# Kernel optimization log

Measured on AMD Instinct MI355X. Metric: run time of the kernel, lower is better.

Reference implementation:

```python
import jax, jax.numpy as jnp
import numpy as np

V, E, H, M = 256, 512, 512, 128
D = 2 * H  # decoder hidden
B, L_TXT, T_MEL = 32, 256, 800
EPS = 1e-5


def setup_inputs() -> dict:
    key = jax.random.key(0)
    ks = jax.random.split(key, 24)
    s = 0.02
    inp = {
        'x': jax.random.randint(ks[0], (B, L_TXT), 0, V),
        'text_seq_lens': jax.random.randint(ks[1], (B,), 1, L_TXT + 1),
        'y': jax.random.normal(ks[2], (B, T_MEL, M), jnp.float32),
        'mel_spec_lens': jax.random.randint(ks[3], (B,), 1, T_MEL + 1),
        'emb': jax.random.normal(ks[4], (V, E)) * s,
        'conv1_w': jax.random.normal(ks[5], (E, E, 3)) * s,
        'conv1_b': jnp.zeros((E,)),
        'bn1_g': jnp.ones((E,)), 'bn1_b': jnp.zeros((E,)),
        'conv2_w': jax.random.normal(ks[6], (E, E, 3)) * s,
        'conv2_b': jnp.zeros((E,)),
        'bn2_g': jnp.ones((E,)), 'bn2_b': jnp.zeros((E,)),
        'wih_f': jax.random.normal(ks[7], (4 * H, E)) * s,
        'whh_f': jax.random.normal(ks[8], (4 * H, H)) * s,
        'bih_f': jnp.zeros((4 * H,)), 'bhh_f': jnp.zeros((4 * H,)),
        'wih_b': jax.random.normal(ks[9], (4 * H, E)) * s,
        'whh_b': jax.random.normal(ks[10], (4 * H, H)) * s,
        'bih_b': jnp.zeros((4 * H,)), 'bhh_b': jnp.zeros((4 * H,)),
        'dwih': jax.random.normal(ks[11], (4 * D, M)) * s,
        'dwhh': jax.random.normal(ks[12], (4 * D, D)) * s,
        'dbih': jnp.zeros((4 * D,)), 'dbhh': jnp.zeros((4 * D,)),
        'proj_w': jax.random.normal(ks[13], (M, D)) * s,
        'proj_b': jnp.zeros((M,)),
        'gate_w': jax.random.normal(ks[14], (1, D)) * s,
        'gate_b': jnp.zeros((1,)),
    }
    return inp


def _conv_bn_relu(x, w, b, g, beta):
    # x: (B, E, L); training-mode BatchNorm (batch statistics, biased var)
    x = jax.lax.conv_general_dilated(x, w, (1,), [(1, 1)],
                                     dimension_numbers=('NCH', 'OIH', 'NCH')) + b[None, :, None]
    mu = jnp.mean(x, axis=(0, 2), keepdims=True)
    var = jnp.mean((x - mu) ** 2, axis=(0, 2), keepdims=True)
    x = (x - mu) * jax.lax.rsqrt(var + EPS) * g[None, :, None] + beta[None, :, None]
    return jax.nn.relu(x)


def _lstm_last(xseq, lens, wih, whh, bih, bhh):
    # Run LSTM over full padded seq, freezing state past each length.
    # Returns final (h, c) == state at t = len-1 (packed-sequence semantics).
    Bb, T, _ = xseq.shape
    Hh = whh.shape[1]
    pre = jnp.einsum('bte,ge->btg', xseq, wih) + bih + bhh  # (B,T,4H)

    def step(carry, inp):
        h, c = carry
        xt, t = inp
        gates = xt + h @ whh.T
        i, f, g, o = jnp.split(gates, 4, axis=-1)
        c_n = jax.nn.sigmoid(f) * c + jax.nn.sigmoid(i) * jnp.tanh(g)
        h_n = jax.nn.sigmoid(o) * jnp.tanh(c_n)
        valid = (t < lens)[:, None]
        return (jnp.where(valid, h_n, h), jnp.where(valid, c_n, c)), None

    init = (jnp.zeros((Bb, Hh), xseq.dtype), jnp.zeros((Bb, Hh), xseq.dtype))
    (h, c), _ = jax.lax.scan(step, init, (pre.transpose(1, 0, 2), jnp.arange(T)))
    return h, c


def _forward(x, text_seq_lens, y, mel_spec_lens, emb, conv1_w, conv1_b, bn1_g, bn1_b,
             conv2_w, conv2_b, bn2_g, bn2_b, wih_f, whh_f, bih_f, bhh_f,
             wih_b, whh_b, bih_b, bhh_b, dwih, dwhh, dbih, dbhh,
             proj_w, proj_b, gate_w, gate_b):
    xe = emb[x]                       # (B, L, E)
    h = xe.transpose(0, 2, 1)         # (B, E, L)
    h = _conv_bn_relu(h, conv1_w, conv1_b, bn1_g, bn1_b)  # dropout = identity (eval)
    h = _conv_bn_relu(h, conv2_w, conv2_b, bn2_g, bn2_b)
    h = h.transpose(0, 2, 1)          # (B, L, E)

    # bidirectional encoder LSTM final states (packed semantics)
    hf, cf = _lstm_last(h, text_seq_lens, wih_f, whh_f, bih_f, bhh_f)
    # reverse each sequence within its valid length for the backward direction
    t_idx = jnp.arange(h.shape[1])[None, :]
    rev_idx = jnp.clip(text_seq_lens[:, None] - 1 - t_idx, 0, h.shape[1] - 1)
    h_rev = jnp.take_along_axis(h, rev_idx[:, :, None], axis=1)
    hb, cb = _lstm_last(h_rev, text_seq_lens, wih_b, whh_b, bih_b, bhh_b)

    hid = jnp.concatenate([hf, hb], axis=1)  # (B, 2H)
    cel = jnp.concatenate([cf, cb], axis=1)

    Tm = y.shape[1]

    def dec_step(carry, _):
        hd, cd, inp = carry
        gates = inp @ dwih.T + dbih + dbhh + hd @ dwhh.T
        i, f, g, o = jnp.split(gates, 4, axis=-1)
        cd = jax.nn.sigmoid(f) * cd + jax.nn.sigmoid(i) * jnp.tanh(g)
        hd = jax.nn.sigmoid(o) * jnp.tanh(cd)
        mel = hd @ proj_w.T + proj_b          # (B, M)
        gate = hd @ gate_w.T + gate_b         # (B, 1)
        return (hd, cd, mel), (mel, gate[:, 0])

    sos = jnp.zeros((y.shape[0], M), y.dtype)
    _, (mels, gates) = jax.lax.scan(dec_step, (hid, cel, sos), None, length=Tm)
    mel_outputs = mels.transpose(1, 0, 2)     # (B, Tm, M)
    gate_outputs = gates.T                    # (B, Tm)

    mask = jnp.arange(Tm)[None, :] > mel_spec_lens[:, None]  # (B, Tm), strictly >
    masked_mel = jnp.where(mask[:, :, None], 0.0, mel_outputs)
    masked_gate = jnp.where(mask, 1000.0, gate_outputs)
    return masked_mel, masked_gate, mask


def reference(x, text_seq_lens, y, mel_spec_lens, emb, conv1_w, conv1_b, bn1_g, bn1_b,
              conv2_w, conv2_b, bn2_g, bn2_b, wih_f, whh_f, bih_f, bhh_f,
              wih_b, whh_b, bih_b, bhh_b, dwih, dwhh, dbih, dbhh,
              proj_w, proj_b, gate_w, gate_b):
    return _forward(x, text_seq_lens, y, mel_spec_lens, emb, conv1_w, conv1_b,
                    bn1_g, bn1_b, conv2_w, conv2_b, bn2_g, bn2_b,
                    wih_f, whh_f, bih_f, bhh_f, wih_b, whh_b, bih_b, bhh_b,
                    dwih, dwhh, dbih, dbhh, proj_w, proj_b, gate_w, gate_b)
```

## Files before the change

kernel.cpp:

```cpp
#include <hip/hip_runtime.h>


typedef float f4 __attribute__((ext_vector_type(4)));
typedef _Float16 h8 __attribute__((ext_vector_type(8)));
typedef _Float16 half_t;
typedef unsigned u4 __attribute__((ext_vector_type(4)));
typedef unsigned long long u64;

#define B_    32
#define LTXT  256
#define TMEL  800
#define EE    512
#define HH    512
#define DD    1024
#define MM    128
#define NROWS 8192
#define GATE_OFF 3276800
#define MASK_OFF 3302400

#define RING_D 101
#define RING_E 33
#define HOP    13

#define WS_MBE        0ull
#define WS_MBD        16384ull
#define WS_HENC       49152ull
#define WS_ZERO_BYTES 114688ull
#define WS_HD         2211840ull
#define WS_BUFX       8830976ull
#define WS_BUFY       17219584ull
#define WS_CONVF      25608192ull
#define WS_WEFF       25608192ull
#define WS_W0         33996800ull
#define WS_WP1        42385408ull
#define WS_WP2        43958272ull
#define WS_WIHP       45531136ull
#define WS_WHHP       49725440ull
#define WS_BSUM       53919744ull
#define WS_BEFF       53936128ull
#define WS_B0         53952512ull
#define WS_MEAN       53968896ull
#define WS_RSTD       53970944ull
#define WS_PROJW      53972992ull
#define WS_PROJG      54235136ull
#define WS_CEL        54267904ull

__device__ __forceinline__ float sigm(float x) { return 1.f / (1.f + __expf(-x)); }
__device__ __forceinline__ float tanh_f(float x) {
    float e = __expf(2.f * x);
    return 1.f - 2.f / (e + 1.f);
}

__device__ __forceinline__ void st_atom64(void* p, u64 v) {
    asm volatile("global_atomic_swap_x2 %0, %1, off" :: "v"(p), "v"(v) : "memory");
}
__device__ __forceinline__ void st_atom32(unsigned* p, unsigned v) {
    asm volatile("global_atomic_swap %0, %1, off" :: "v"(p), "v"(v) : "memory");
}
__device__ __forceinline__ u4 ld_l3(const void* p) {
    u4 r;
    asm volatile("global_load_dwordx4 %0, %1, off sc0 sc1" : "=v"(r) : "v"(p) : "memory");
    return r;
}
__device__ __forceinline__ void wait_vm0() {
    asm volatile("s_waitcnt vmcnt(0)" ::: "memory");
    __builtin_amdgcn_sched_barrier(0);
}


__global__ void k_embed(const int* __restrict__ x, const float* __restrict__ emb,
                        half_t* __restrict__ out) {
    int row = blockIdx.x;
    int tok = x[row];
    const float* e = emb + (size_t)tok * EE;
    half_t* o = out + (size_t)row * EE;
    for (int c = threadIdx.x; c < EE; c += blockDim.x) o[c] = (half_t)e[c];
}

__global__ void k_packconvw(const float* __restrict__ w, half_t* __restrict__ wp) {
    int idx = blockIdx.x * 256 + threadIdx.x;
    if (idx >= 3 * EE * EE) return;
    int s = idx / (EE * EE);
    int rem = idx - s * EE * EE;
    int eo = rem >> 9, ei = rem & 511;
    wp[idx] = (half_t)w[(size_t)eo * (EE * 3) + ei * 3 + s];
}

__global__ __launch_bounds__(256) void k_conv(const half_t* __restrict__ A,
                                              const half_t* __restrict__ Wp,
                                              const float* __restrict__ bias,
                                              float* __restrict__ out) {
    const int nt = blockIdx.x, et = blockIdx.y;
    const int tid = threadIdx.x;
    const int wv = tid >> 6, l = tid & 63, quad = l >> 4, lo = l & 15;
    const int rowA = nt * 64 + wv * 16 + lo;
    const int eo = et * 16 + lo;
    f4 acc = {0.f, 0.f, 0.f, 0.f};
    for (int s = 0; s < 3; ++s) {
        int lsp = (rowA & 255) + s - 1;
        bool valid = (lsp >= 0) && (lsp < 256);
        int rs = rowA + s - 1;
        rs = rs < 0 ? 0 : (rs > NROWS - 1 ? NROWS - 1 : rs);
        const half_t* ab = A + (size_t)rs * EE;
        const half_t* wb = Wp + ((size_t)s * EE + eo) * EE;
#pragma unroll 4
        for (int ks = 0; ks < 16; ++ks) {
            h8 a = {0, 0, 0, 0, 0, 0, 0, 0};
            if (valid) a = *(const h8*)(ab + ks * 32 + quad * 8);
            h8 b = *(const h8*)(wb + ks * 32 + quad * 8);
            acc = __builtin_amdgcn_mfma_f32_16x16x32_f16(a, b, acc, 0, 0, 0);
        }
    }
    const int orow = nt * 64 + wv * 16 + quad * 4;
    const float bv = bias[eo];
#pragma unroll
    for (int r = 0; r < 4; ++r) out[(size_t)(orow + r) * EE + eo] = acc[r] + bv;
}

__global__ __launch_bounds__(256) void k_bnstats(const float* __restrict__ x,
                                                 float* __restrict__ mean,
                                                 float* __restrict__ rstd) {
    const int c = blockIdx.x;
    float s = 0.f, ss = 0.f;
    for (int n = threadIdx.x; n < NROWS; n += 256) {
        float v = x[(size_t)n * EE + c];
        s += v; ss += v * v;
    }
#pragma unroll
    for (int off = 32; off > 0; off >>= 1) { s += __shfl_down(s, off); ss += __shfl_down(ss, off); }
    __shared__ float as[4], ass[4];
    int wv = threadIdx.x >> 6;
    if ((threadIdx.x & 63) == 0) { as[wv] = s; ass[wv] = ss; }
    __syncthreads();
    if (threadIdx.x == 0) {
        float S = as[0] + as[1] + as[2] + as[3];
        float SS = ass[0] + ass[1] + ass[2] + ass[3];
        float m = S / (float)NROWS;
        float var = SS / (float)NROWS - m * m;
        mean[c] = m;
        rstd[c] = rsqrtf(var + 1e-5f);
    }
}

__global__ void k_bnapply(const float* __restrict__ x, const float* __restrict__ mean,
                          const float* __restrict__ rstd, const float* __restrict__ g,
                          const float* __restrict__ beta, half_t* __restrict__ out) {
    int idx = blockIdx.x * 256 + threadIdx.x;
    if (idx >= NROWS * EE) return;
    int c = idx & (EE - 1);
    float v = (x[idx] - mean[c]) * rstd[c] * g[c] + beta[c];
    out[idx] = (half_t)(v > 0.f ? v : 0.f);
}

__global__ void k_packrec(const float* __restrict__ src, half_t* __restrict__ dst,
                          int Hdim, int kshift, int total) {
    int idx = blockIdx.x * 256 + threadIdx.x;
    if (idx >= total) return;
    int p = idx >> kshift;
    int k = idx & ((1 << kshift) - 1);
    int he = p >> 2, g = p & 3;
    dst[idx] = (half_t)src[((size_t)g * Hdim + he) * (size_t)(1 << kshift) + k];
}

__global__ void k_bsumenc(const float* __restrict__ bf, const float* __restrict__ bhf,
                          const float* __restrict__ bb, const float* __restrict__ bhb,
                          float* __restrict__ bsum) {
    int p = blockIdx.x * 256 + threadIdx.x;
    if (p >= 4096) return;
    int dir = p >> 11, pp = p & 2047;
    int he = pp >> 2, g = pp & 3;
    int row = g * HH + he;
    bsum[p] = dir ? (bb[row] + bhb[row]) : (bf[row] + bhf[row]);
}

__global__ __launch_bounds__(256) void k_weff(const float* __restrict__ dwhh,
                                              const float* __restrict__ dwih,
                                              const float* __restrict__ projw,
                                              half_t* __restrict__ weff,
                                              half_t* __restrict__ w0) {
    int row = blockIdx.x;
    int k = blockIdx.y * 256 + threadIdx.x;
    float v = dwhh[(size_t)row * DD + k];
    float acc = v;
    for (int m = 0; m < MM; ++m) acc += dwih[(size_t)row * MM + m] * projw[(size_t)m * DD + k];
    int p = ((row & (DD - 1)) << 2) | (row >> 10);
    weff[(size_t)p * DD + k] = (half_t)acc;
    w0[(size_t)p * DD + k] = (half_t)v;
}

__global__ void k_bdec(const float* __restrict__ dbih, const float* __restrict__ dbhh,
                       const float* __restrict__ dwih, const float* __restrict__ projb,
                       float* __restrict__ beff, float* __restrict__ b0) {
    int p = blockIdx.x * 256 + threadIdx.x;
    if (p >= 4096) return;
    int he = p >> 2, g = p & 3;
    int row = g * DD + he;
    float bb = dbih[row] + dbhh[row];
    float acc = bb;
    for (int m = 0; m < MM; ++m) acc += dwih[(size_t)row * MM + m] * projb[m];
    b0[p] = bb;
    beff[p] = acc;
}

__global__ void k_cast(const float* __restrict__ src, half_t* __restrict__ dst, int n) {
    int idx = blockIdx.x * 256 + threadIdx.x;
    if (idx < n) dst[idx] = (half_t)src[idx];
}

__global__ void k_projg(const float* __restrict__ gw, half_t* __restrict__ pg) {
    int idx = blockIdx.x * 256 + threadIdx.x;
    if (idx >= 16 * DD) return;
    int row = idx >> 10, k = idx & (DD - 1);
    pg[idx] = (half_t)(row == 0 ? gw[k] : 0.f);
}

__global__ void k_mask(const int* __restrict__ lens, float* __restrict__ out) {
    int idx = blockIdx.x * 256 + threadIdx.x;
    if (idx >= B_ * TMEL) return;
    int b = idx / TMEL, t = idx - b * TMEL;
    out[MASK_OFF + idx] = (t > lens[b]) ? 1.f : 0.f;
}

__global__ __launch_bounds__(512) void k_enc(const half_t* __restrict__ X,
                                             const half_t* __restrict__ wihp,
                                             const half_t* __restrict__ whhp,
                                             const float* __restrict__ bsum,
                                             const int* __restrict__ lens,
                                             half_t* __restrict__ henc,
                                             half_t* __restrict__ hd0,
                                             float* __restrict__ cel,
                                             unsigned* __restrict__ mbE) {
    const int j = blockIdx.x;
    const int dir = j >> 5, sub = j & 31;
    const int tid = threadIdx.x;
    const int wv = tid >> 6, l = tid & 63, quad = l >> 4, lo = l & 15;
    const int rg = wv >> 1, bh = wv & 1;
    const int bfr = bh * 16 + lo;
    const int ue = tid >> 5, ub = tid & 31;

    __shared__ half_t s_hd[32 * 520];
    __shared__ float s_g[32][65];
    __shared__ float s_c[16][32];
    __shared__ float s_h[16][32];
    __shared__ half_t s_hh[16][32];
    __shared__ int s_len[32];

    if (tid < 32) s_len[tid] = lens[tid];
    s_c[ue][ub] = 0.f;
    s_h[ue][ub] = 0.f;

    const int pr = dir * 2048 + sub * 64 + rg * 16 + lo;
    const half_t* wih_b = wihp + (size_t)pr * 512;
    const half_t* whh_b = whhp + (size_t)pr * 512;
    const float bias_n = bsum[pr];

    h8 wihreg[16], whhreg[16];
#pragma unroll
    for (int ks = 0; ks < 16; ++ks) {
        wihreg[ks] = *(const h8*)(wih_b + ks * 32 + quad * 8);
        whhreg[ks] = *(const h8*)(whh_b + ks * 32 + quad * 8);
    }

    int sp = 0, sn = HOP;
    __syncthreads();

    for (int t = 0; t < 256; ++t) {
        if (t > 0) {
            if (tid >= 64 && tid < 96) {
                const unsigned want = (unsigned)t;
                const unsigned* fp = mbE + (size_t)(dir * 32 + sub) * 64 + (tid - 64);
                while (__hip_atomic_load(fp, __ATOMIC_RELAXED, __HIP_MEMORY_SCOPE_AGENT) < want)
                    __builtin_amdgcn_s_sleep(1);
            }
            __syncthreads();
        }

        const half_t* src = henc + (size_t)sp * 32768 + (size_t)dir * 16384;
        u4 tmp0 = ld_l3(src + (size_t)(tid + 0 * 512) * 8);
        u4 tmp1 = ld_l3(src + (size_t)(tid + 1 * 512) * 8);
        u4 tmp2 = ld_l3(src + (size_t)(tid + 2 * 512) * 8);
        u4 tmp3 = ld_l3(src + (size_t)(tid + 3 * 512) * 8);

        const int lb = s_len[bfr];
        int tt = (dir == 0) ? t : (lb - 1 - t);
        tt = tt < 0 ? 0 : tt;
        const half_t* xr = X + ((size_t)bfr * 256 + tt) * 512;
        f4 accA = {0.f, 0.f, 0.f, 0.f}, accB = {0.f, 0.f, 0.f, 0.f};
#pragma unroll
        for (int ks = 0; ks < 16; ++ks) {
            h8 a = *(const h8*)(xr + ks * 32 + quad * 8);
            accA = __builtin_amdgcn_mfma_f32_16x16x32_f16(a, wihreg[ks], accA, 0, 0, 0);
        }

        wait_vm0();
        {
            int c0 = tid;
            *(u4*)(s_hd + (size_t)(c0 >> 6) * 520 + (c0 & 63) * 8) = tmp0;
            int c1 = tid + 512;
            *(u4*)(s_hd + (size_t)(c1 >> 6) * 520 + (c1 & 63) * 8) = tmp1;
            int c2 = tid + 1024;
            *(u4*)(s_hd + (size_t)(c2 >> 6) * 520 + (c2 & 63) * 8) = tmp2;
            int c3 = tid + 1536;
            *(u4*)(s_hd + (size_t)(c3 >> 6) * 520 + (c3 & 63) * 8) = tmp3;
        }
        __syncthreads();

#pragma unroll
        for (int ks = 0; ks < 16; ++ks) {
            h8 a = *(const h8*)(s_hd + (size_t)bfr * 520 + ks * 32 + quad * 8);
            accB = __builtin_amdgcn_mfma_f32_16x16x32_f16(a, whhreg[ks], accB, 0, 0, 0);
        }
        const int bm = bh * 16 + quad * 4, cm = rg * 16 + lo;
#pragma unroll
        for (int r = 0; r < 4; ++r) s_g[bm + r][cm] = accA[r] + accB[r] + bias_n;
        __syncthreads();
        {
            float gi = s_g[ub][ue * 4 + 0], gf = s_g[ub][ue * 4 + 1];
            float gg = s_g[ub][ue * 4 + 2], go = s_g[ub][ue * 4 + 3];
            float cn = sigm(gf) * s_c[ue][ub] + sigm(gi) * tanh_f(gg);
            float hn = sigm(go) * tanh_f(cn);
            if (t < s_len[ub]) { s_c[ue][ub] = cn; s_h[ue][ub] = hn; }
            s_hh[ue][ub] = (half_t)s_h[ue][ub];
        }
        __syncthreads();
        if (tid < 64 && t < 255) {
            int b2 = tid >> 1, e8 = (tid & 1) * 8;
            union { half_t h[8]; u64 u[2]; } pk;
#pragma unroll
            for (int i = 0; i < 8; ++i) pk.h[i] = s_hh[e8 + i][b2];
            half_t* dst = henc + (size_t)sn * 32768 + (size_t)dir * 16384
                          + (size_t)b2 * 512 + sub * 16 + e8;
            st_atom64(dst, pk.u[0]);
            st_atom64(dst + 4, pk.u[1]);
            asm volatile("s_waitcnt vmcnt(0)");
            if (tid < 32)
                st_atom32(mbE + ((size_t)(dir * 32 + tid) * 64 + sub), (unsigned)(t + 1));
        }
        if (t < 255) { sp = sn; sn += HOP; if (sn >= RING_E) sn -= RING_E; }
    }
    hd0[(size_t)ub * 1024 + dir * 512 + sub * 16 + ue] = (half_t)s_h[ue][ub];
    cel[(size_t)ub * 1024 + dir * 512 + sub * 16 + ue] = s_c[ue][ub];
}

__global__ __launch_bounds__(512) void k_dec(const half_t* __restrict__ Weff,
                                             const half_t* __restrict__ W0,
                                             const float* __restrict__ beff,
                                             const float* __restrict__ b0,
                                             const half_t* __restrict__ projwb,
                                             const half_t* __restrict__ projg,
                                             const float* __restrict__ projb,
                                             const float* __restrict__ gateb,
                                             const int* __restrict__ mlens,
                                             const float* __restrict__ cel,
                                             half_t* __restrict__ hd,
                                             float* __restrict__ out,
                                             unsigned* __restrict__ mbD) {
    const int j = blockIdx.x;
    const int tid = threadIdx.x;
    const int wv = tid >> 6, l = tid & 63, quad = l >> 4, lo = l & 15;

    __shared__ half_t s_hd[32 * 1032];
    __shared__ float s_g[32][65];
    __shared__ float s_c[16][32];
    __shared__ half_t s_hh[16][32];
    __shared__ int s_len[32];

    if (j < 64) {
        const int rg = wv >> 1, bh = wv & 1;
        const int bfr = bh * 16 + lo;
        const int ue = tid >> 5, ub = tid & 31;

        s_c[ue][ub] = cel[(size_t)ub * 1024 + j * 16 + ue];
        const int pr = j * 64 + rg * 16 + lo;
        const float biasE = beff[pr], bias0 = b0[pr];
        const half_t* wbE = Weff + (size_t)pr * 1024;
        const half_t* wb0 = W0 + (size_t)pr * 1024;

        h8 wreg[32];
#pragma unroll
        for (int ks = 0; ks < 32; ++ks)
            wreg[ks] = *(const h8*)(wbE + ks * 32 + quad * 8);

        int sp = 0, sn = HOP;
        __syncthreads();

        for (int t = 1; t <= TMEL; ++t) {
            if (t > 1) {
                if (tid >= 64 && tid < 128) {
                    const unsigned want = (unsigned)(t - 1);
                    const unsigned* fp = mbD + (size_t)j * 64 + (tid - 64);
                    while (__hip_atomic_load(fp, __ATOMIC_RELAXED, __HIP_MEMORY_SCOPE_AGENT) < want)
                        __builtin_amdgcn_s_sleep(1);
                }
                __syncthreads();
            }

            {
                const half_t* src = hd + (size_t)sp * 32768;
                u4 tp[8];
#pragma unroll
                for (int i = 0; i < 8; ++i)
                    tp[i] = ld_l3(src + (size_t)(tid + i * 512) * 8);
                wait_vm0();
#pragma unroll
                for (int i = 0; i < 8; ++i) {
                    int c = tid + i * 512;
                    *(u4*)(s_hd + (size_t)(c >> 7) * 1032 + (c & 127) * 8) = tp[i];
                }
            }
            __syncthreads();

            const half_t* ar = s_hd + (size_t)bfr * 1032 + quad * 8;
            f4 acc = {0.f, 0.f, 0.f, 0.f}, acc2 = {0.f, 0.f, 0.f, 0.f};
            if (t == 1) {
#pragma unroll 8
                for (int ks = 0; ks < 32; ks += 2) {
                    h8 a0 = *(const h8*)(ar + ks * 32);
                    h8 a1 = *(const h8*)(ar + ks * 32 + 32);
                    acc = __builtin_amdgcn_mfma_f32_16x16x32_f16(a0, *(const h8*)(wb0 + ks * 32 + quad * 8), acc, 0, 0, 0);
                    acc2 = __builtin_amdgcn_mfma_f32_16x16x32_f16(a1, *(const h8*)(wb0 + ks * 32 + 32 + quad * 8), acc2, 0, 0, 0);
                }
            } else {
#pragma unroll
                for (int ks = 0; ks < 32; ks += 2) {
                    h8 a0 = *(const h8*)(ar + ks * 32);
                    h8 a1 = *(const h8*)(ar + ks * 32 + 32);
                    acc = __builtin_amdgcn_mfma_f32_16x16x32_f16(a0, wreg[ks], acc, 0, 0, 0);
                    acc2 = __builtin_amdgcn_mfma_f32_16x16x32_f16(a1, wreg[ks + 1], acc2, 0, 0, 0);
                }
            }
            const float bn = (t == 1) ? bias0 : biasE;
            const int bm = bh * 16 + quad * 4, cm = rg * 16 + lo;
#pragma unroll
            for (int r = 0; r < 4; ++r) s_g[bm + r][cm] = acc[r] + acc2[r] + bn;
            __syncthreads();
            {
                float gi = s_g[ub][ue * 4 + 0], gf = s_g[ub][ue * 4 + 1];
                float gg = s_g[ub][ue * 4 + 2], go = s_g[ub][ue * 4 + 3];
                float cn = sigm(gf) * s_c[ue][ub] + sigm(gi) * tanh_f(gg);
                s_c[ue][ub] = cn;
                s_hh[ue][ub] = (half_t)(sigm(go) * tanh_f(cn));
            }
            __syncthreads();
            if (tid < 64) {
                int b2 = tid >> 1, e8 = (tid & 1) * 8;
                union { half_t h[8]; u64 u[2]; } pk;
#pragma unroll
                for (int i = 0; i < 8; ++i) pk.h[i] = s_hh[e8 + i][b2];
                half_t* dst = hd + (size_t)sn * 32768 + (size_t)b2 * 1024 + j * 16 + e8;
                st_atom64(dst, pk.u[0]);
                st_atom64(dst + 4, pk.u[1]);
                asm volatile("s_waitcnt vmcnt(0)");
                st_atom32(mbD + ((size_t)tid * 64 + j), (unsigned)t);
                if (tid < 9)
                    st_atom32(mbD + ((size_t)(64 + tid) * 64 + j), (unsigned)t);
            }
            sp = sn; sn += HOP; if (sn >= RING_D) sn -= RING_D;
        }
    } else {
        const int pj = j - 64;
        const bool meld = (pj < 8);
        const bool duty = (wv < 2);
        const int bh2 = wv & 1;
        const half_t* pw = meld ? (projwb + (size_t)(pj * 16 + lo) * 1024)
                                : (projg + (size_t)lo * 1024);
        const float biasP = meld ? projb[pj * 16 + lo] : gateb[0];

        h8 pwreg[32];
        if (duty) {
#pragma unroll
            for (int ks = 0; ks < 32; ++ks)
                pwreg[ks] = *(const h8*)(pw + ks * 32 + quad * 8);
        }
        if (tid < 32) s_len[tid] = mlens[tid];

        int spP = HOP;
        __syncthreads();

        for (int t = 1; t <= TMEL; ++t) {
            if (tid < 64) {
                const unsigned want = (unsigned)t;
                const unsigned* fp = mbD + (size_t)(64 + pj) * 64 + tid;
                while (__hip_atomic_load(fp, __ATOMIC_RELAXED, __HIP_MEMORY_SCOPE_AGENT) < want)
                    __builtin_amdgcn_s_sleep(1);
            }
            __syncthreads();

            {
                const half_t* src = hd + (size_t)spP * 32768;
                u4 tp[8];
#pragma unroll
                for (int i = 0; i < 8; ++i)
                    tp[i] = ld_l3(src + (size_t)(tid + i * 512) * 8);
                wait_vm0();
#pragma unroll
                for (int i = 0; i < 8; ++i) {
                    int c = tid + i * 512;
                    *(u4*)(s_hd + (size_t)(c >> 7) * 1032 + (c & 127) * 8) = tp[i];
                }
            }
            __syncthreads();

            if (duty) {
                const half_t* ar = s_hd + (size_t)(bh2 * 16 + lo) * 1032 + quad * 8;
                f4 accm = {0.f, 0.f, 0.f, 0.f}, accm2 = {0.f, 0.f, 0.f, 0.f};
#pragma unroll
                for (int ks = 0; ks < 32; ks += 2) {
                    h8 a0 = *(const h8*)(ar + ks * 32);
                    h8 a1 = *(const h8*)(ar + ks * 32 + 32);
                    accm = __builtin_amdgcn_mfma_f32_16x16x32_f16(a0, pwreg[ks], accm, 0, 0, 0);
                    accm2 = __builtin_amdgcn_mfma_f32_16x16x32_f16(a1, pwreg[ks + 1], accm2, 0, 0, 0);
                }
                accm[0] += accm2[0]; accm[1] += accm2[1];
                accm[2] += accm2[2]; accm[3] += accm2[3];
                const int pos = t - 1;
                if (meld) {
#pragma unroll
                    for (int r = 0; r < 4; ++r) {
                        int b = bh2 * 16 + quad * 4 + r;
                        float v = accm[r] + biasP;
                        if (pos > s_len[b]) v = 0.f;
                        __builtin_nontemporal_store(v,
                            &out[(size_t)b * (TMEL * MM) + (size_t)pos * MM + pj * 16 + lo]);
                    }
                } else if (lo == 0) {
#pragma unroll
                    for (int r = 0; r < 4; ++r) {
                        int b = bh2 * 16 + quad * 4 + r;
                        float v = accm[r] + biasP;
                        if (pos > s_len[b]) v = 1000.f;
                        __builtin_nontemporal_store(v, &out[GATE_OFF + (size_t)b * TMEL + pos]);
                    }
                }
            }
            __syncthreads();
            spP += HOP; if (spP >= RING_D) spP -= RING_D;
        }
    }
}


extern "C" void kernel_launch(void* const* d_in, const int* in_sizes, int n_in,
                              void* d_out, int out_size, void* d_ws, size_t ws_size,
                              hipStream_t stream) {
    const int* x = (const int*)d_in[0];
    const int* tlens = (const int*)d_in[1];
    const int* mlens = (const int*)d_in[3];
    const float* emb = (const float*)d_in[4];
    const float* c1w = (const float*)d_in[5];
    const float* c1b = (const float*)d_in[6];
    const float* bn1g = (const float*)d_in[7];
    const float* bn1b = (const float*)d_in[8];
    const float* c2w = (const float*)d_in[9];
    const float* c2b = (const float*)d_in[10];
    const float* bn2g = (const float*)d_in[11];
    const float* bn2b = (const float*)d_in[12];
    const float* wihf = (const float*)d_in[13];
    const float* whhf = (const float*)d_in[14];
    const float* bihf = (const float*)d_in[15];
    const float* bhhf = (const float*)d_in[16];
    const float* wihb = (const float*)d_in[17];
    const float* whhb = (const float*)d_in[18];
    const float* bihb = (const float*)d_in[19];
    const float* bhhb = (const float*)d_in[20];
    const float* dwih = (const float*)d_in[21];
    const float* dwhh = (const float*)d_in[22];
    const float* dbih = (const float*)d_in[23];
    const float* dbhh = (const float*)d_in[24];
    const float* projw = (const float*)d_in[25];
    const float* projb = (const float*)d_in[26];
    const float* gatew = (const float*)d_in[27];
    const float* gateb = (const float*)d_in[28];
    float* out = (float*)d_out;
    char* ws = (char*)d_ws;

    unsigned* mbE = (unsigned*)(ws + WS_MBE);
    unsigned* mbD = (unsigned*)(ws + WS_MBD);
    half_t* henc = (half_t*)(ws + WS_HENC);
    half_t* hd = (half_t*)(ws + WS_HD);
    half_t* bufX = (half_t*)(ws + WS_BUFX);
    half_t* bufY = (half_t*)(ws + WS_BUFY);
    float* convf = (float*)(ws + WS_CONVF);
    half_t* weff = (half_t*)(ws + WS_WEFF);
    half_t* w0 = (half_t*)(ws + WS_W0);
    half_t* wp1 = (half_t*)(ws + WS_WP1);
    half_t* wp2 = (half_t*)(ws + WS_WP2);
    float* meanb = (float*)(ws + WS_MEAN);
    float* rstdb = (float*)(ws + WS_RSTD);
    half_t* wihp = (half_t*)(ws + WS_WIHP);
    half_t* whhp = (half_t*)(ws + WS_WHHP);
    float* bsum = (float*)(ws + WS_BSUM);
    float* beff = (float*)(ws + WS_BEFF);
    float* b0 = (float*)(ws + WS_B0);
    half_t* projwb = (half_t*)(ws + WS_PROJW);
    half_t* projg = (half_t*)(ws + WS_PROJG);
    float* cel = (float*)(ws + WS_CEL);

    hipMemsetAsync(d_ws, 0, (size_t)WS_ZERO_BYTES, stream);

    k_embed<<<NROWS, 256, 0, stream>>>(x, emb, bufX);
    k_packconvw<<<(3 * EE * EE + 255) / 256, 256, 0, stream>>>(c1w, wp1);
    k_conv<<<dim3(128, 32), 256, 0, stream>>>(bufX, wp1, c1b, convf);
    k_bnstats<<<EE, 256, 0, stream>>>(convf, meanb, rstdb);
    k_bnapply<<<(NROWS * EE) / 256, 256, 0, stream>>>(convf, meanb, rstdb, bn1g, bn1b, bufY);
    k_packconvw<<<(3 * EE * EE + 255) / 256, 256, 0, stream>>>(c2w, wp2);
    k_conv<<<dim3(128, 32), 256, 0, stream>>>(bufY, wp2, c2b, convf);
    k_bnstats<<<EE, 256, 0, stream>>>(convf, meanb, rstdb);
    k_bnapply<<<(NROWS * EE) / 256, 256, 0, stream>>>(convf, meanb, rstdb, bn2g, bn2b, bufX);

    const int encTot = 2048 * 512;
    k_packrec<<<(encTot + 255) / 256, 256, 0, stream>>>(wihf, wihp, HH, 9, encTot);
    k_packrec<<<(encTot + 255) / 256, 256, 0, stream>>>(wihb, wihp + encTot, HH, 9, encTot);
    k_packrec<<<(encTot + 255) / 256, 256, 0, stream>>>(whhf, whhp, HH, 9, encTot);
    k_packrec<<<(encTot + 255) / 256, 256, 0, stream>>>(whhb, whhp + encTot, HH, 9, encTot);
    k_bsumenc<<<16, 256, 0, stream>>>(bihf, bhhf, bihb, bhhb, bsum);

    k_enc<<<64, 512, 0, stream>>>(bufX, wihp, whhp, bsum, tlens, henc, hd, cel, mbE);

    k_weff<<<dim3(4096, 4), 256, 0, stream>>>(dwhh, dwih, projw, weff, w0);
    k_bdec<<<16, 256, 0, stream>>>(dbih, dbhh, dwih, projb, beff, b0);
    k_cast<<<(MM * DD + 255) / 256, 256, 0, stream>>>(projw, projwb, MM * DD);
    k_projg<<<(16 * DD + 255) / 256, 256, 0, stream>>>(gatew, projg);

    k_dec<<<73, 512, 0, stream>>>(weff, w0, beff, b0, projwb, projg, projb, gateb,
                                  mlens, cel, hd, out, mbD);

    k_mask<<<(B_ * TMEL + 255) / 256, 256, 0, stream>>>(mlens, out);

    (void)in_sizes; (void)n_in; (void)out_size; (void)ws_size;
}
```

Baseline: 5.149 ms.

## Replace mailbox flags with epoch-tagged data words in recurrent ring buffers

The encoder and decoder recurrences now embed an epoch/timestep tag beside every 32-bit pair of hidden-state halves, and consumers spin directly on the data words. This replaces the separate per-block mailbox flags, the store-then-flag ordering wait, and the extra barrier round. The decoder's backpressure is now an explicit progress counter from the projection blocks, and ring sizes are reduced. The cost is doubling the bytes moved per step for the hidden state, plus per-element polling loops. A per-launch epoch counter avoids clearing the large ring buffers on every call.

After: 12.49 ms. 2.43x slower.

```diff
diff --git a/kernel.cpp b/kernel.cpp
--- a/kernel.cpp
+++ b/kernel.cpp
@@ -18,38 +18,41 @@
 #define GATE_OFF 3276800
 #define MASK_OFF 3302400
 
-#define RING_D 101
-#define RING_E 33
+#define RING_D 64
+#define RING_E 16
 #define HOP    13
 
-#define WS_MBE        0ull
-#define WS_MBD        16384ull
-#define WS_HENC       49152ull
-#define WS_ZERO_BYTES 114688ull
-#define WS_HD         2211840ull
-#define WS_BUFX       8830976ull
-#define WS_BUFY       17219584ull
-#define WS_CONVF      25608192ull
-#define WS_WEFF       25608192ull
-#define WS_W0         33996800ull
-#define WS_WP1        42385408ull
-#define WS_WP2        43958272ull
-#define WS_WIHP       45531136ull
-#define WS_WHHP       49725440ull
-#define WS_BSUM       53919744ull
-#define WS_BEFF       53936128ull
-#define WS_B0         53952512ull
-#define WS_MEAN       53968896ull
-#define WS_RSTD       53970944ull
-#define WS_PROJW      53972992ull
-#define WS_PROJG      54235136ull
-#define WS_CEL        54267904ull
+#define WS_PROG       0ull
+#define WS_EPOCT      4096ull
+#define WS_EPOCH      4160ull
+#define WS_HENC       8192ull
+#define WS_HD         2105344ull
+#define WS_BUFX       10493952ull
+#define WS_BUFY       18882560ull
+#define WS_CONVF      27271168ull
+#define WS_WEFF       27271168ull
+#define WS_W0         35659776ull
+#define WS_WP1        44048384ull
+#define WS_WP2        45621248ull
+#define WS_WIHP       47194112ull
+#define WS_WHHP       51388416ull
+#define WS_BSUM       55582720ull
+#define WS_BEFF       55599104ull
+#define WS_B0         55615488ull
+#define WS_MEAN       55631872ull
+#define WS_RSTD       55633920ull
+#define WS_PROJW      55635968ull
+#define WS_PROJG      55898112ull
+#define WS_CEL        55930880ull
 
 __device__ __forceinline__ float sigm(float x) { return 1.f / (1.f + __expf(-x)); }
 __device__ __forceinline__ float tanh_f(float x) {
     float e = __expf(2.f * x);
     return 1.f - 2.f / (e + 1.f);
 }
+__device__ __forceinline__ unsigned mktag(unsigned ep, int t) {
+    return (ep << 11) | (unsigned)t;
+}
 
 __device__ __forceinline__ void st_atom64(void* p, u64 v) {
     asm volatile("global_atomic_swap_x2 %0, %1, off" :: "v"(p), "v"(v) : "memory");
@@ -67,6 +70,12 @@
     __builtin_amdgcn_sched_barrier(0);
 }
 
+
+__global__ void k_epoch(unsigned long long* ctr, unsigned* cur) {
+    unsigned long long e = *ctr + 1ull;
+    *ctr = e;
+    *cur = (unsigned)e;
+}
 
 __global__ void k_embed(const int* __restrict__ x, const float* __restrict__ emb,
                         half_t* __restrict__ out) {
@@ -226,10 +235,10 @@
                                              const half_t* __restrict__ whhp,
                                              const float* __restrict__ bsum,
                                              const int* __restrict__ lens,
-                                             half_t* __restrict__ henc,
-                                             half_t* __restrict__ hd0,
+                                             u64* __restrict__ hencT,
+                                             u64* __restrict__ hdT,
                                              float* __restrict__ cel,
-                                             unsigned* __restrict__ mbE) {
+                                             const unsigned* __restrict__ epc) {
     const int j = blockIdx.x;
     const int dir = j >> 5, sub = j & 31;
     const int tid = threadIdx.x;
@@ -248,6 +257,7 @@
     if (tid < 32) s_len[tid] = lens[tid];
     s_c[ue][ub] = 0.f;
     s_h[ue][ub] = 0.f;
+    const unsigned ep = epc[0];
 
     const int pr = dir * 2048 + sub * 64 + rg * 16 + lo;
     const half_t* wih_b = wihp + (size_t)pr * 512;
@@ -265,21 +275,11 @@
     __syncthreads();
 
     for (int t = 0; t < 256; ++t) {
-        if (t > 0) {
-            if (tid >= 64 && tid < 96) {
-                const unsigned want = (unsigned)t;
-                const unsigned* fp = mbE + (size_t)(dir * 32 + sub) * 64 + (tid - 64);
-                while (__hip_atomic_load(fp, __ATOMIC_RELAXED, __HIP_MEMORY_SCOPE_AGENT) < want)
-                    __builtin_amdgcn_s_sleep(1);
-            }
-            __syncthreads();
-        }
-
-        const half_t* src = henc + (size_t)sp * 32768 + (size_t)dir * 16384;
-        u4 tmp0 = ld_l3(src + (size_t)(tid + 0 * 512) * 8);
-        u4 tmp1 = ld_l3(src + (size_t)(tid + 1 * 512) * 8);
-        u4 tmp2 = ld_l3(src + (size_t)(tid + 2 * 512) * 8);
-        u4 tmp3 = ld_l3(src + (size_t)(tid + 3 * 512) * 8);
+        const char* base = (const char*)hencT + (size_t)sp * 131072 + (size_t)dir * 65536;
+        u4 tp[8];
+#pragma unroll
+        for (int i = 0; i < 8; ++i)
+            tp[i] = ld_l3(base + ((size_t)tid + i * 512) * 16);
 
         const int lb = s_len[bfr];
         int tt = (dir == 0) ? t : (lb - 1 - t);
@@ -293,15 +293,22 @@
         }
 
         wait_vm0();
-        {
-            int c0 = tid;
-            *(u4*)(s_hd + (size_t)(c0 >> 6) * 520 + (c0 & 63) * 8) = tmp0;
-            int c1 = tid + 512;
-            *(u4*)(s_hd + (size_t)(c1 >> 6) * 520 + (c1 & 63) * 8) = tmp1;
-            int c2 = tid + 1024;
-            *(u4*)(s_hd + (size_t)(c2 >> 6) * 520 + (c2 & 63) * 8) = tmp2;
-            int c3 = tid + 1536;
-            *(u4*)(s_hd + (size_t)(c3 >> 6) * 520 + (c3 & 63) * 8) = tmp3;
+        if (t > 0) {
+            const unsigned want = mktag(ep, t);
+#pragma unroll
+            for (int i = 0; i < 8; ++i) {
+                while (tp[i][1] != want || tp[i][3] != want) {
+                    __builtin_amdgcn_s_sleep(4);
+                    tp[i] = ld_l3(base + ((size_t)tid + i * 512) * 16);
+                    wait_vm0();
+                }
+            }
+        }
+#pragma unroll
+        for (int i = 0; i < 8; ++i) {
+            int pp = tid + i * 512;
+            u64 v = ((u64)tp[i][2] << 32) | (u64)tp[i][0];
+            *(u64*)(s_hd + (size_t)(pp >> 7) * 520 + (pp & 127) * 4) = v;
         }
         __syncthreads();
 
@@ -324,21 +331,25 @@
         }
         __syncthreads();
         if (tid < 64 && t < 255) {
-            int b2 = tid >> 1, e8 = (tid & 1) * 8;
-            union { half_t h[8]; u64 u[2]; } pk;
-#pragma unroll
-            for (int i = 0; i < 8; ++i) pk.h[i] = s_hh[e8 + i][b2];
-            half_t* dst = henc + (size_t)sn * 32768 + (size_t)dir * 16384
-                          + (size_t)b2 * 512 + sub * 16 + e8;
-            st_atom64(dst, pk.u[0]);
-            st_atom64(dst + 4, pk.u[1]);
-            asm volatile("s_waitcnt vmcnt(0)");
-            if (tid < 32)
-                st_atom32(mbE + ((size_t)(dir * 32 + tid) * 64 + sub), (unsigned)(t + 1));
+            int b2 = tid >> 1, hv = tid & 1;
+            const u64 tagw = (u64)mktag(ep, t + 1) << 32;
+            u64* dstw = hencT + (size_t)sn * 16384 + (size_t)dir * 8192
+                        + (size_t)b2 * 256 + sub * 8 + hv * 4;
+#pragma unroll
+            for (int k = 0; k < 4; ++k) {
+                int e = hv * 8 + 2 * k;
+                union { half_t h[2]; unsigned u; } pk;
+                pk.h[0] = s_hh[e + 0][b2]; pk.h[1] = s_hh[e + 1][b2];
+                st_atom64(dstw + k, tagw | (u64)pk.u);
+            }
         }
         if (t < 255) { sp = sn; sn += HOP; if (sn >= RING_E) sn -= RING_E; }
     }
-    hd0[(size_t)ub * 1024 + dir * 512 + sub * 16 + ue] = (half_t)s_h[ue][ub];
+    if (!(ue & 1)) {
+        union { half_t h[2]; unsigned u; } pk;
+        pk.h[0] = (half_t)s_h[ue][ub]; pk.h[1] = (half_t)s_h[ue + 1][ub];
+        hdT[(size_t)ub * 512 + dir * 256 + sub * 8 + (ue >> 1)] = (u64)pk.u;
+    }
     cel[(size_t)ub * 1024 + dir * 512 + sub * 16 + ue] = s_c[ue][ub];
 }
 
@@ -352,12 +363,14 @@
                                              const float* __restrict__ gateb,
                                              const int* __restrict__ mlens,
                                              const float* __restrict__ cel,
-                                             half_t* __restrict__ hd,
+                                             u64* __restrict__ hdT,
                                              float* __restrict__ out,
-                                             unsigned* __restrict__ mbD) {
+                                             unsigned* __restrict__ prog,
+                                             const unsigned* __restrict__ epc) {
     const int j = blockIdx.x;
     const int tid = threadIdx.x;
     const int wv = tid >> 6, l = tid & 63, quad = l >> 4, lo = l & 15;
+    const unsigned ep = epc[0];
 
     __shared__ half_t s_hd[32 * 1032];
     __shared__ float s_g[32][65];
@@ -385,28 +398,31 @@
         __syncthreads();
 
         for (int t = 1; t <= TMEL; ++t) {
+            const char* base = (const char*)hdT + (size_t)sp * 131072;
+            u4 tp[16];
+#pragma unroll
+            for (int i = 0; i < 16; ++i)
+                tp[i] = ld_l3(base + ((size_t)tid + i * 512) * 16);
+            unsigned pv = 0x7FFFFFFFu;
+            if (tid < 9)
+                pv = __hip_atomic_load(prog + tid, __ATOMIC_RELAXED, __HIP_MEMORY_SCOPE_AGENT);
+            wait_vm0();
             if (t > 1) {
-                if (tid >= 64 && tid < 128) {
-                    const unsigned want = (unsigned)(t - 1);
-                    const unsigned* fp = mbD + (size_t)j * 64 + (tid - 64);
-                    while (__hip_atomic_load(fp, __ATOMIC_RELAXED, __HIP_MEMORY_SCOPE_AGENT) < want)
-                        __builtin_amdgcn_s_sleep(1);
-                }
-                __syncthreads();
-            }
-
-            {
-                const half_t* src = hd + (size_t)sp * 32768;
-                u4 tp[8];
-#pragma unroll
-                for (int i = 0; i < 8; ++i)
-                    tp[i] = ld_l3(src + (size_t)(tid + i * 512) * 8);
-                wait_vm0();
-#pragma unroll
-                for (int i = 0; i < 8; ++i) {
-                    int c = tid + i * 512;
-                    *(u4*)(s_hd + (size_t)(c >> 7) * 1032 + (c & 127) * 8) = tp[i];
-                }
+                const unsigned want = mktag(ep, t - 1);
+#pragma unroll
+                for (int i = 0; i < 16; ++i) {
+                    while (tp[i][1] != want || tp[i][3] != want) {
+                        __builtin_amdgcn_s_sleep(4);
+                        tp[i] = ld_l3(base + ((size_t)tid + i * 512) * 16);
+                        wait_vm0();
+                    }
+                }
+            }
+#pragma unroll
+            for (int i = 0; i < 16; ++i) {
+                int pp = tid + i * 512;
+                u64 v = ((u64)tp[i][2] << 32) | (u64)tp[i][0];
+                *(u64*)(s_hd + (size_t)(pp >> 8) * 1032 + (pp & 255) * 4) = v;
             }
             __syncthreads();
 
@@ -443,17 +459,25 @@
             }
             __syncthreads();
             if (tid < 64) {
-                int b2 = tid >> 1, e8 = (tid & 1) * 8;
-                union { half_t h[8]; u64 u[2]; } pk;
-#pragma unroll
-                for (int i = 0; i < 8; ++i) pk.h[i] = s_hh[e8 + i][b2];
-                half_t* dst = hd + (size_t)sn * 32768 + (size_t)b2 * 1024 + j * 16 + e8;
-                st_atom64(dst, pk.u[0]);
-                st_atom64(dst + 4, pk.u[1]);
-                asm volatile("s_waitcnt vmcnt(0)");
-                st_atom32(mbD + ((size_t)tid * 64 + j), (unsigned)t);
-                if (tid < 9)
-                    st_atom32(mbD + ((size_t)(64 + tid) * 64 + j), (unsigned)t);
+                if (t >= 63) {
+                    const int need = t - 62;
+                    while (!__all((int)pv >= need)) {
+                        __builtin_amdgcn_s_sleep(8);
+                        if (tid < 9)
+                            pv = __hip_atomic_load(prog + tid, __ATOMIC_RELAXED,
+                                                   __HIP_MEMORY_SCOPE_AGENT);
+                    }
+                }
+                int b2 = tid >> 1, hv = tid & 1;
+                const u64 tagw = (u64)mktag(ep, t) << 32;
+                u64* dstw = hdT + (size_t)sn * 16384 + (size_t)b2 * 512 + j * 8 + hv * 4;
+#pragma unroll
+                for (int k = 0; k < 4; ++k) {
+                    int e = hv * 8 + 2 * k;
+                    union { half_t h[2]; unsigned u; } pk;
+                    pk.h[0] = s_hh[e + 0][b2]; pk.h[1] = s_hh[e + 1][b2];
+                    st_atom64(dstw + k, tagw | (u64)pk.u);
+                }
             }
             sp = sn; sn += HOP; if (sn >= RING_D) sn -= RING_D;
         }
@@ -478,26 +502,28 @@
         __syncthreads();
 
         for (int t = 1; t <= TMEL; ++t) {
-            if (tid < 64) {
-                const unsigned want = (unsigned)t;
-                const unsigned* fp = mbD + (size_t)(64 + pj) * 64 + tid;
-                while (__hip_atomic_load(fp, __ATOMIC_RELAXED, __HIP_MEMORY_SCOPE_AGENT) < want)
-                    __builtin_amdgcn_s_sleep(1);
-            }
-            __syncthreads();
-
+            const char* base = (const char*)hdT + (size_t)spP * 131072;
+            u4 tp[16];
+#pragma unroll
+            for (int i = 0; i < 16; ++i)
+                tp[i] = ld_l3(base + ((size_t)tid + i * 512) * 16);
+            wait_vm0();
             {
-                const half_t* src = hd + (size_t)spP * 32768;
-                u4 tp[8];
-#pragma unroll
-                for (int i = 0; i < 8; ++i)
-                    tp[i] = ld_l3(src + (size_t)(tid + i * 512) * 8);
-                wait_vm0();
-#pragma unroll
-                for (int i = 0; i < 8; ++i) {
-                    int c = tid + i * 512;
-                    *(u4*)(s_hd + (size_t)(c >> 7) * 1032 + (c & 127) * 8) = tp[i];
-                }
+                const unsigned want = mktag(ep, t);
+#pragma unroll
+                for (int i = 0; i < 16; ++i) {
+                    while (tp[i][1] != want || tp[i][3] != want) {
+                        __builtin_amdgcn_s_sleep(4);
+                        tp[i] = ld_l3(base + ((size_t)tid + i * 512) * 16);
+                        wait_vm0();
+                    }
+                }
+            }
+#pragma unroll
+            for (int i = 0; i < 16; ++i) {
+                int pp = tid + i * 512;
+                u64 v = ((u64)tp[i][2] << 32) | (u64)tp[i][0];
+                *(u64*)(s_hd + (size_t)(pp >> 8) * 1032 + (pp & 255) * 4) = v;
             }
             __syncthreads();
 
@@ -534,6 +560,7 @@
                 }
             }
             __syncthreads();
+            if (tid == 0) st_atom32(prog + pj, (unsigned)t);
             spP += HOP; if (spP >= RING_D) spP -= RING_D;
         }
     }
@@ -574,10 +601,11 @@
     float* out = (float*)d_out;
     char* ws = (char*)d_ws;
 
-    unsigned* mbE = (unsigned*)(ws + WS_MBE);
-    unsigned* mbD = (unsigned*)(ws + WS_MBD);
-    half_t* henc = (half_t*)(ws + WS_HENC);
-    half_t* hd = (half_t*)(ws + WS_HD);
+    unsigned* prog = (unsigned*)(ws + WS_PROG);
+    unsigned long long* epoct = (unsigned long long*)(ws + WS_EPOCT);
+    unsigned* epc = (unsigned*)(ws + WS_EPOCH);
+    u64* hencT = (u64*)(ws + WS_HENC);
+    u64* hdT = (u64*)(ws + WS_HD);
     half_t* bufX = (half_t*)(ws + WS_BUFX);
     half_t* bufY = (half_t*)(ws + WS_BUFY);
     float* convf = (float*)(ws + WS_CONVF);
@@ -596,7 +624,9 @@
     half_t* projg = (half_t*)(ws + WS_PROJG);
     float* cel = (float*)(ws + WS_CEL);
 
-    hipMemsetAsync(d_ws, 0, (size_t)WS_ZERO_BYTES, stream);
+    hipMemsetAsync(ws + WS_PROG, 0, 4096, stream);
+    hipMemsetAsync(ws + WS_HENC, 0, 131072, stream);
+    k_epoch<<<1, 1, 0, stream>>>(epoct, epc);
 
     k_embed<<<NROWS, 256, 0, stream>>>(x, emb, bufX);
     k_packconvw<<<(3 * EE * EE + 255) / 256, 256, 0, stream>>>(c1w, wp1);
@@ -615,7 +645,7 @@
     k_packrec<<<(encTot + 255) / 256, 256, 0, stream>>>(whhb, whhp + encTot, HH, 9, encTot);
     k_bsumenc<<<16, 256, 0, stream>>>(bihf, bhhf, bihb, bhhb, bsum);
 
-    k_enc<<<64, 512, 0, stream>>>(bufX, wihp, whhp, bsum, tlens, henc, hd, cel, mbE);
+    k_enc<<<64, 512, 0, stream>>>(bufX, wihp, whhp, bsum, tlens, hencT, hdT, cel, epc);
 
     k_weff<<<dim3(4096, 4), 256, 0, stream>>>(dwhh, dwih, projw, weff, w0);
     k_bdec<<<16, 256, 0, stream>>>(dbih, dbhh, dwih, projb, beff, b0);
@@ -623,7 +653,7 @@
     k_projg<<<(16 * DD + 255) / 256, 256, 0, stream>>>(gatew, projg);
 
     k_dec<<<73, 512, 0, stream>>>(weff, w0, beff, b0, projwb, projg, projb, gateb,
-                                  mlens, cel, hd, out, mbD);
+                                  mlens, cel, hdT, out, prog, epc);
 
     k_mask<<<(B_ * TMEL + 255) / 256, 256, 0, stream>>>(mlens, out);
 
```
